# Performance work log

Measured on AMD Instinct MI355X. Metric: run time of the kernel, lower is better.

Reference implementation:

```python
import jax, jax.numpy as jnp
import numpy as np

TOP_K = 2

def setup_inputs() -> dict:
    key = jax.random.key(0)
    k1, k2 = jax.random.split(key)
    B, S, D, E = 4, 8192, 1024, 64
    hidden_states = jax.random.normal(k1, (B, S, D), dtype=jnp.float32)
    gate_weight = jax.random.normal(k2, (E, D), dtype=jnp.float32) * (1.0 / D ** 0.5)
    return {"hidden_states": hidden_states, "gate_weight": gate_weight}

def reference(hidden_states, gate_weight):
    # router_logits: [B, S, E] = hidden @ W^T
    router_logits = jnp.einsum('bsd,ed->bse', hidden_states, gate_weight)
    # softmax in float32 (matches .float() in torch), cast back to input dtype
    router_probs = jax.nn.softmax(router_logits.astype(jnp.float32), axis=-1).astype(hidden_states.dtype)
    top_k_probs, selected_experts = jax.lax.top_k(router_probs, TOP_K)
    top_k_probs = top_k_probs / (jnp.sum(top_k_probs, axis=-1, keepdims=True) + 1e-08)
    return top_k_probs, selected_experts, router_logits
```

## Files before the change

### kernel.cpp

```cpp
#include <hip/hip_runtime.h>
#include <math.h>


typedef __attribute__((ext_vector_type(8))) short bf16x8;
typedef __attribute__((ext_vector_type(4))) float f32x4;

static constexpr int TOKENS = 32768;
static constexpr int DDIM   = 1024;
static constexpr int NEXP   = 64;
static constexpr size_t OFF_EXP = 65536;
static constexpr size_t OFF_LOG = 131072;

__global__ void w_split3_kernel(const float* __restrict__ w,
                                short* __restrict__ w1,
                                short* __restrict__ w2,
                                short* __restrict__ w3) {
    int idx = blockIdx.x * blockDim.x + threadIdx.x;
    for (int i = idx; i < NEXP * DDIM; i += gridDim.x * blockDim.x) {
        int e = i >> 10, k = i & 1023;
        float f = w[i];
        unsigned u1 = __float_as_uint(f);
        float f1 = __uint_as_float(u1 & 0xffff0000u);
        float r1 = f - f1;
        unsigned u2 = __float_as_uint(r1);
        float f2 = __uint_as_float(u2 & 0xffff0000u);
        float r2 = r1 - f2;
        unsigned u3 = __float_as_uint(r2);
        int n = e >> 4, c = k >> 5;
        int lane = (e & 15) + ((k & 31) >> 3) * 16;
        int j = k & 7;
        size_t dst = ((size_t)(c * 4 + n) * 64 + lane) * 8 + j;
        w1[dst] = (short)(u1 >> 16);
        w2[dst] = (short)(u2 >> 16);
        w3[dst] = (short)(u3 >> 16);
    }
}

__device__ inline void split8(float4 a, float4 b,
                              bf16x8& o1, bf16x8& o2, bf16x8& o3) {
    float f[8] = {a.x, a.y, a.z, a.w, b.x, b.y, b.z, b.w};
#pragma unroll
    for (int j = 0; j < 8; ++j) {
        unsigned u1 = __float_as_uint(f[j]);
        float f1 = __uint_as_float(u1 & 0xffff0000u);
        float r1 = f[j] - f1;
        unsigned u2 = __float_as_uint(r1);
        float f2 = __uint_as_float(u2 & 0xffff0000u);
        float r2 = r1 - f2;
        o1[j] = (short)(u1 >> 16);
        o2[j] = (short)(u2 >> 16);
        o3[j] = (short)(__float_as_uint(r2) >> 16);
    }
}

typedef const __attribute__((address_space(1))) unsigned int* gas1_t;
typedef __attribute__((address_space(3))) unsigned int* las3_t;
__device__ inline void stage16(const void* g, void* l) {
    __builtin_amdgcn_global_load_lds((gas1_t)(uintptr_t)g,
                                     (las3_t)(uintptr_t)l, 16, 0, 0);
}

__global__ __launch_bounds__(512, 2)
void router_mfma_kernel(const float* __restrict__ h,
                        const short* __restrict__ w1,
                        const short* __restrict__ w2,
                        const short* __restrict__ w3,
                        float* __restrict__ out) {
    __shared__ alignas(16) char smem[73728];
    const int tid   = threadIdx.x;
    const int lane  = tid & 63;
    const int wv    = tid >> 6;
    const int khalf = wv & 1;
    const int mg    = wv >> 1;
    const int token0 = blockIdx.x * 128 + mg * 32;
    const int arow  = lane & 15;
    const int ks    = lane >> 4;

    const float* ap0 = h + (size_t)(token0 + arow) * DDIM + khalf * 512 + ks * 8;
    const float* ap1 = ap0 + (size_t)16 * DDIM;

    const short* warr[3] = {w1, w2, w3};
    const char* gsrc[3];
    int ldso[3];
#pragma unroll
    for (int i = 0; i < 3; ++i) {
        int seg = wv * 3 + i;
        int kh = seg & 1;
        int an = seg >> 1;
        int a = an >> 2, n = an & 3;
        gsrc[i] = (const char*)warr[a] + (size_t)(kh * 64 + n) * 1024 + lane * 16;
        ldso[i] = (kh * 12 + a * 4 + n) * 1024;
    }

#define STAGE(bb, cc)                                                      \
    {                                                                      \
        _Pragma("unroll")                                                  \
        for (int i = 0; i < 3; ++i)                                        \
            stage16(gsrc[i] + (size_t)(cc) * 4096,                         \
                    smem + (bb) * 24576 + ldso[i]);                        \
    }

    f32x4 acc[2][4];
#pragma unroll
    for (int m = 0; m < 2; ++m)
#pragma unroll
        for (int n = 0; n < 4; ++n)
#pragma unroll
            for (int r = 0; r < 4; ++r) acc[m][n][r] = 0.0f;

    float4 ringA[2][2][2];

    ringA[0][0][0] = *reinterpret_cast<const float4*>(ap0);
    ringA[0][0][1] = *reinterpret_cast<const float4*>(ap0 + 4);
    ringA[0][1][0] = *reinterpret_cast<const float4*>(ap1);
    ringA[0][1][1] = *reinterpret_cast<const float4*>(ap1 + 4);
    STAGE(0, 0);
    STAGE(1, 1);
    asm volatile("s_waitcnt vmcnt(3)" ::: "memory");
    __builtin_amdgcn_s_barrier();

#pragma unroll
    for (int t = 0; t < 16; ++t) {
        const int slot  = t & 1;
        const int nslot = slot ^ 1;
        if (t + 1 < 16) {
            ringA[nslot][0][0] =
                *reinterpret_cast<const float4*>(ap0 + (t + 1) * 32);
            ringA[nslot][0][1] =
                *reinterpret_cast<const float4*>(ap0 + (t + 1) * 32 + 4);
            ringA[nslot][1][0] =
                *reinterpret_cast<const float4*>(ap1 + (t + 1) * 32);
            ringA[nslot][1][1] =
                *reinterpret_cast<const float4*>(ap1 + (t + 1) * 32 + 4);
        }
        if (t + 2 < 16) STAGE((t + 2) % 3, t + 2);

        bf16x8 A1a, A2a, A3a, A1b, A2b, A3b;
        split8(ringA[slot][0][0], ringA[slot][0][1], A1a, A2a, A3a);
        split8(ringA[slot][1][0], ringA[slot][1][1], A1b, A2b, A3b);

        const char* wb = smem + (t % 3) * 24576 + khalf * 12288 + lane * 16;
#pragma unroll
        for (int n = 0; n < 4; ++n) {
            bf16x8 W1v = *reinterpret_cast<const bf16x8*>(wb + n * 1024);
            bf16x8 W2v = *reinterpret_cast<const bf16x8*>(wb + n * 1024 + 4096);
            bf16x8 W3v = *reinterpret_cast<const bf16x8*>(wb + n * 1024 + 8192);
            f32x4 t0 = acc[0][n];
            t0 = __builtin_amdgcn_mfma_f32_16x16x32_bf16(A3a, W1v, t0, 0, 0, 0);
            t0 = __builtin_amdgcn_mfma_f32_16x16x32_bf16(A1a, W3v, t0, 0, 0, 0);
            t0 = __builtin_amdgcn_mfma_f32_16x16x32_bf16(A2a, W2v, t0, 0, 0, 0);
            t0 = __builtin_amdgcn_mfma_f32_16x16x32_bf16(A2a, W1v, t0, 0, 0, 0);
            t0 = __builtin_amdgcn_mfma_f32_16x16x32_bf16(A1a, W2v, t0, 0, 0, 0);
            t0 = __builtin_amdgcn_mfma_f32_16x16x32_bf16(A1a, W1v, t0, 0, 0, 0);
            acc[0][n] = t0;
            f32x4 t1 = acc[1][n];
            t1 = __builtin_amdgcn_mfma_f32_16x16x32_bf16(A3b, W1v, t1, 0, 0, 0);
            t1 = __builtin_amdgcn_mfma_f32_16x16x32_bf16(A1b, W3v, t1, 0, 0, 0);
            t1 = __builtin_amdgcn_mfma_f32_16x16x32_bf16(A2b, W2v, t1, 0, 0, 0);
            t1 = __builtin_amdgcn_mfma_f32_16x16x32_bf16(A2b, W1v, t1, 0, 0, 0);
            t1 = __builtin_amdgcn_mfma_f32_16x16x32_bf16(A1b, W2v, t1, 0, 0, 0);
            t1 = __builtin_amdgcn_mfma_f32_16x16x32_bf16(A1b, W1v, t1, 0, 0, 0);
            acc[1][n] = t1;
        }

        if (t <= 13) {
            asm volatile("s_waitcnt vmcnt(7)" ::: "memory");
            __builtin_amdgcn_s_barrier();
        } else if (t == 14) {
            asm volatile("s_waitcnt vmcnt(4)" ::: "memory");
            __builtin_amdgcn_s_barrier();
        }
    }

    if (khalf == 1) {
        float* cb = (float*)(smem + 24576) + (size_t)(mg * 64 + lane) * 33;
#pragma unroll
        for (int m = 0; m < 2; ++m)
#pragma unroll
            for (int n = 0; n < 4; ++n)
#pragma unroll
                for (int r = 0; r < 4; ++r)
                    cb[m * 16 + n * 4 + r] = acc[m][n][r];
    }
    __syncthreads();
    if (khalf != 0) return;

    {
        const float* cb = (const float*)(smem + 24576)
                        + (size_t)(mg * 64 + lane) * 33;
#pragma unroll
        for (int m = 0; m < 2; ++m)
#pragma unroll
            for (int n = 0; n < 4; ++n)
#pragma unroll
                for (int r = 0; r < 4; ++r)
                    acc[m][n][r] += cb[m * 16 + n * 4 + r];
    }

    const int rbase = (lane >> 4) * 4;
    const int col   = lane & 15;

#pragma unroll
    for (int m = 0; m < 2; ++m)
#pragma unroll
        for (int n = 0; n < 4; ++n)
#pragma unroll
            for (int r = 0; r < 4; ++r)
                out[OFF_LOG + (size_t)(token0 + m * 16 + rbase + r) * NEXP
                    + n * 16 + col] = acc[m][n][r];

#pragma unroll
    for (int m = 0; m < 2; ++m)
#pragma unroll
    for (int r = 0; r < 4; ++r) {
        const int token = token0 + m * 16 + rbase + r;
        float mx = fmaxf(fmaxf(acc[m][0][r], acc[m][1][r]),
                         fmaxf(acc[m][2][r], acc[m][3][r]));
#pragma unroll
        for (int d = 1; d <= 8; d <<= 1) mx = fmaxf(mx, __shfl_xor(mx, d, 64));

        float p[4];
        float s = 0.0f;
#pragma unroll
        for (int n = 0; n < 4; ++n) { p[n] = expf(acc[m][n][r] - mx); s += p[n]; }
#pragma unroll
        for (int d = 1; d <= 8; d <<= 1) s += __shfl_xor(s, d, 64);

        float v1 = -INFINITY, v2 = -INFINITY;
        int   i1 = NEXP,      i2 = NEXP;
#pragma unroll
        for (int n = 0; n < 4; ++n) {
            float v = p[n];
            int   ei = n * 16 + col;
            if (v > v1)      { v2 = v1; i2 = i1; v1 = v; i1 = ei; }
            else if (v > v2) { v2 = v;  i2 = ei; }
        }

#pragma unroll
        for (int d = 1; d <= 8; d <<= 1) {
            float ov1 = __shfl_xor(v1, d, 64);
            float ov2 = __shfl_xor(v2, d, 64);
            int   oi1 = __shfl_xor(i1, d, 64);
            int   oi2 = __shfl_xor(i2, d, 64);
            bool ofirst = (ov1 > v1) || (ov1 == v1 && oi1 < i1);
            float n1, n2; int ni1, ni2;
            if (ofirst) {
                n1 = ov1; ni1 = oi1;
                bool sec = (v1 > ov2) || (v1 == ov2 && i1 < oi2);
                n2 = sec ? v1 : ov2; ni2 = sec ? i1 : oi2;
            } else {
                n1 = v1; ni1 = i1;
                bool sec = (ov1 > v2) || (ov1 == v2 && oi1 < i2);
                n2 = sec ? ov1 : v2; ni2 = sec ? oi1 : i2;
            }
            v1 = n1; i1 = ni1; v2 = n2; i2 = ni2;
        }

        if (col == 0) {
            float t1 = v1 / s;
            float t2 = v2 / s;
            float dn = t1 + t2 + 1e-8f;
            float2 pr; pr.x = t1 / dn; pr.y = t2 / dn;
            *reinterpret_cast<float2*>(out + (size_t)token * 2) = pr;
            float2 ex; ex.x = (float)i1; ex.y = (float)i2;
            *reinterpret_cast<float2*>(out + OFF_EXP + (size_t)token * 2) = ex;
        }
    }
#undef STAGE
}

extern "C" void kernel_launch(void* const* d_in, const int* in_sizes, int n_in,
                              void* d_out, int out_size, void* d_ws, size_t ws_size,
                              hipStream_t stream) {
    const float* h = (const float*)d_in[0];
    const float* w = (const float*)d_in[1];
    float* out = (float*)d_out;
    short* w1 = (short*)d_ws;
    short* w2 = w1 + (size_t)NEXP * DDIM;
    short* w3 = w2 + (size_t)NEXP * DDIM;
    hipLaunchKernelGGL(w_split3_kernel, dim3(128), dim3(256), 0, stream, w, w1, w2, w3);
    hipLaunchKernelGGL(router_mfma_kernel, dim3(TOKENS / 128), dim3(512), 0, stream,
                       h, w1, w2, w3, out);
}
```

Measured before the change: 52.07 us.

## Split expert columns across waves and halve tokens per block

Each block now handles 64 tokens instead of 128. The waves are split three ways: by k-half, by expert half (ng), and by token group. This halves the accumulator registers per wave, and launch bounds are raised to request more resident blocks. The activation prefetch ring is deepened from two to three stages, aligned with the weight staging. The price is an extra LDS reduction round with a second barrier to gather the expert halves. Each weight stage is now loaded into LDS for every 64 tokens rather than every 128, doubling weight staging traffic.

```diff
diff --git a/kernel.cpp b/kernel.cpp
--- a/kernel.cpp
+++ b/kernel.cpp
@@ -60,7 +60,7 @@
                                      (las3_t)(uintptr_t)l, 16, 0, 0);
 }
 
-__global__ __launch_bounds__(512, 2)
+__global__ __launch_bounds__(512, 4)
 void router_mfma_kernel(const float* __restrict__ h,
                         const short* __restrict__ w1,
                         const short* __restrict__ w2,
@@ -71,8 +71,9 @@
     const int lane  = tid & 63;
     const int wv    = tid >> 6;
     const int khalf = wv & 1;
-    const int mg    = wv >> 1;
-    const int token0 = blockIdx.x * 128 + mg * 32;
+    const int ng    = (wv >> 1) & 1;
+    const int mg    = wv >> 2;
+    const int token0 = blockIdx.x * 64 + mg * 32;
     const int arow  = lane & 15;
     const int ks    = lane >> 4;
 
@@ -100,101 +101,129 @@
                     smem + (bb) * 24576 + ldso[i]);                        \
     }
 
-    f32x4 acc[2][4];
+    f32x4 acc[2][2];
 #pragma unroll
     for (int m = 0; m < 2; ++m)
 #pragma unroll
-        for (int n = 0; n < 4; ++n)
-#pragma unroll
-            for (int r = 0; r < 4; ++r) acc[m][n][r] = 0.0f;
-
-    float4 ringA[2][2][2];
-
-    ringA[0][0][0] = *reinterpret_cast<const float4*>(ap0);
-    ringA[0][0][1] = *reinterpret_cast<const float4*>(ap0 + 4);
-    ringA[0][1][0] = *reinterpret_cast<const float4*>(ap1);
-    ringA[0][1][1] = *reinterpret_cast<const float4*>(ap1 + 4);
+        for (int nl = 0; nl < 2; ++nl)
+#pragma unroll
+            for (int r = 0; r < 4; ++r) acc[m][nl][r] = 0.0f;
+
+    float4 ring[3][2][2];
+
     STAGE(0, 0);
     STAGE(1, 1);
-    asm volatile("s_waitcnt vmcnt(3)" ::: "memory");
+    ring[0][0][0] = *reinterpret_cast<const float4*>(ap0);
+    ring[0][0][1] = *reinterpret_cast<const float4*>(ap0 + 4);
+    ring[0][1][0] = *reinterpret_cast<const float4*>(ap1);
+    ring[0][1][1] = *reinterpret_cast<const float4*>(ap1 + 4);
+    ring[1][0][0] = *reinterpret_cast<const float4*>(ap0 + 32);
+    ring[1][0][1] = *reinterpret_cast<const float4*>(ap0 + 36);
+    ring[1][1][0] = *reinterpret_cast<const float4*>(ap1 + 32);
+    ring[1][1][1] = *reinterpret_cast<const float4*>(ap1 + 36);
+    asm volatile("s_waitcnt vmcnt(0)" ::: "memory");
     __builtin_amdgcn_s_barrier();
 
 #pragma unroll
     for (int t = 0; t < 16; ++t) {
-        const int slot  = t & 1;
-        const int nslot = slot ^ 1;
-        if (t + 1 < 16) {
-            ringA[nslot][0][0] =
-                *reinterpret_cast<const float4*>(ap0 + (t + 1) * 32);
-            ringA[nslot][0][1] =
-                *reinterpret_cast<const float4*>(ap0 + (t + 1) * 32 + 4);
-            ringA[nslot][1][0] =
-                *reinterpret_cast<const float4*>(ap1 + (t + 1) * 32);
-            ringA[nslot][1][1] =
-                *reinterpret_cast<const float4*>(ap1 + (t + 1) * 32 + 4);
-        }
-        if (t + 2 < 16) STAGE((t + 2) % 3, t + 2);
+        if (t + 2 < 16) {
+            STAGE((t + 2) % 3, t + 2);
+            ring[(t + 2) % 3][0][0] =
+                *reinterpret_cast<const float4*>(ap0 + (t + 2) * 32);
+            ring[(t + 2) % 3][0][1] =
+                *reinterpret_cast<const float4*>(ap0 + (t + 2) * 32 + 4);
+            ring[(t + 2) % 3][1][0] =
+                *reinterpret_cast<const float4*>(ap1 + (t + 2) * 32);
+            ring[(t + 2) % 3][1][1] =
+                *reinterpret_cast<const float4*>(ap1 + (t + 2) * 32 + 4);
+        }
 
         bf16x8 A1a, A2a, A3a, A1b, A2b, A3b;
-        split8(ringA[slot][0][0], ringA[slot][0][1], A1a, A2a, A3a);
-        split8(ringA[slot][1][0], ringA[slot][1][1], A1b, A2b, A3b);
-
-        const char* wb = smem + (t % 3) * 24576 + khalf * 12288 + lane * 16;
-#pragma unroll
-        for (int n = 0; n < 4; ++n) {
-            bf16x8 W1v = *reinterpret_cast<const bf16x8*>(wb + n * 1024);
-            bf16x8 W2v = *reinterpret_cast<const bf16x8*>(wb + n * 1024 + 4096);
-            bf16x8 W3v = *reinterpret_cast<const bf16x8*>(wb + n * 1024 + 8192);
-            f32x4 t0 = acc[0][n];
+        split8(ring[t % 3][0][0], ring[t % 3][0][1], A1a, A2a, A3a);
+        split8(ring[t % 3][1][0], ring[t % 3][1][1], A1b, A2b, A3b);
+
+        const char* wb = smem + (t % 3) * 24576 + khalf * 12288
+                       + (ng * 2) * 1024 + lane * 16;
+#pragma unroll
+        for (int nl = 0; nl < 2; ++nl) {
+            bf16x8 W1v = *reinterpret_cast<const bf16x8*>(wb + nl * 1024);
+            bf16x8 W2v = *reinterpret_cast<const bf16x8*>(wb + nl * 1024 + 4096);
+            bf16x8 W3v = *reinterpret_cast<const bf16x8*>(wb + nl * 1024 + 8192);
+            f32x4 t0 = acc[0][nl];
             t0 = __builtin_amdgcn_mfma_f32_16x16x32_bf16(A3a, W1v, t0, 0, 0, 0);
             t0 = __builtin_amdgcn_mfma_f32_16x16x32_bf16(A1a, W3v, t0, 0, 0, 0);
             t0 = __builtin_amdgcn_mfma_f32_16x16x32_bf16(A2a, W2v, t0, 0, 0, 0);
             t0 = __builtin_amdgcn_mfma_f32_16x16x32_bf16(A2a, W1v, t0, 0, 0, 0);
             t0 = __builtin_amdgcn_mfma_f32_16x16x32_bf16(A1a, W2v, t0, 0, 0, 0);
             t0 = __builtin_amdgcn_mfma_f32_16x16x32_bf16(A1a, W1v, t0, 0, 0, 0);
-            acc[0][n] = t0;
-            f32x4 t1 = acc[1][n];
+            acc[0][nl] = t0;
+            f32x4 t1 = acc[1][nl];
             t1 = __builtin_amdgcn_mfma_f32_16x16x32_bf16(A3b, W1v, t1, 0, 0, 0);
             t1 = __builtin_amdgcn_mfma_f32_16x16x32_bf16(A1b, W3v, t1, 0, 0, 0);
             t1 = __builtin_amdgcn_mfma_f32_16x16x32_bf16(A2b, W2v, t1, 0, 0, 0);
             t1 = __builtin_amdgcn_mfma_f32_16x16x32_bf16(A2b, W1v, t1, 0, 0, 0);
             t1 = __builtin_amdgcn_mfma_f32_16x16x32_bf16(A1b, W2v, t1, 0, 0, 0);
             t1 = __builtin_amdgcn_mfma_f32_16x16x32_bf16(A1b, W1v, t1, 0, 0, 0);
-            acc[1][n] = t1;
+            acc[1][nl] = t1;
         }
 
         if (t <= 13) {
             asm volatile("s_waitcnt vmcnt(7)" ::: "memory");
             __builtin_amdgcn_s_barrier();
         } else if (t == 14) {
-            asm volatile("s_waitcnt vmcnt(4)" ::: "memory");
+            asm volatile("s_waitcnt vmcnt(0)" ::: "memory");
             __builtin_amdgcn_s_barrier();
         }
     }
 
     if (khalf == 1) {
-        float* cb = (float*)(smem + 24576) + (size_t)(mg * 64 + lane) * 33;
+        float* cA = (float*)(smem + 24576)
+                  + (size_t)((mg * 2 + ng) * 64 + lane) * 17;
 #pragma unroll
         for (int m = 0; m < 2; ++m)
 #pragma unroll
-            for (int n = 0; n < 4; ++n)
+            for (int nl = 0; nl < 2; ++nl)
 #pragma unroll
                 for (int r = 0; r < 4; ++r)
-                    cb[m * 16 + n * 4 + r] = acc[m][n][r];
+                    cA[(m * 2 + nl) * 4 + r] = acc[m][nl][r];
     }
     __syncthreads();
-    if (khalf != 0) return;
-
+    if (khalf == 0) {
+        const float* cA = (const float*)(smem + 24576)
+                        + (size_t)((mg * 2 + ng) * 64 + lane) * 17;
+#pragma unroll
+        for (int m = 0; m < 2; ++m)
+#pragma unroll
+            for (int nl = 0; nl < 2; ++nl)
+#pragma unroll
+                for (int r = 0; r < 4; ++r)
+                    acc[m][nl][r] += cA[(m * 2 + nl) * 4 + r];
+        if (ng == 1) {
+            float* cB = (float*)smem + (size_t)(mg * 64 + lane) * 17;
+#pragma unroll
+            for (int m = 0; m < 2; ++m)
+#pragma unroll
+                for (int nl = 0; nl < 2; ++nl)
+#pragma unroll
+                    for (int r = 0; r < 4; ++r)
+                        cB[(m * 2 + nl) * 4 + r] = acc[m][nl][r];
+        }
+    }
+    __syncthreads();
+    if (khalf != 0 || ng != 0) return;
+
+    f32x4 acc4[2][4];
     {
-        const float* cb = (const float*)(smem + 24576)
-                        + (size_t)(mg * 64 + lane) * 33;
+        const float* cB = (const float*)smem + (size_t)(mg * 64 + lane) * 17;
 #pragma unroll
         for (int m = 0; m < 2; ++m)
 #pragma unroll
-            for (int n = 0; n < 4; ++n)
+            for (int nl = 0; nl < 2; ++nl) {
+                acc4[m][nl] = acc[m][nl];
 #pragma unroll
                 for (int r = 0; r < 4; ++r)
-                    acc[m][n][r] += cb[m * 16 + n * 4 + r];
+                    acc4[m][2 + nl][r] = cB[(m * 2 + nl) * 4 + r];
+            }
     }
 
     const int rbase = (lane >> 4) * 4;
@@ -207,22 +236,22 @@
 #pragma unroll
             for (int r = 0; r < 4; ++r)
                 out[OFF_LOG + (size_t)(token0 + m * 16 + rbase + r) * NEXP
-                    + n * 16 + col] = acc[m][n][r];
+                    + n * 16 + col] = acc4[m][n][r];
 
 #pragma unroll
     for (int m = 0; m < 2; ++m)
 #pragma unroll
     for (int r = 0; r < 4; ++r) {
         const int token = token0 + m * 16 + rbase + r;
-        float mx = fmaxf(fmaxf(acc[m][0][r], acc[m][1][r]),
-                         fmaxf(acc[m][2][r], acc[m][3][r]));
+        float mx = fmaxf(fmaxf(acc4[m][0][r], acc4[m][1][r]),
+                         fmaxf(acc4[m][2][r], acc4[m][3][r]));
 #pragma unroll
         for (int d = 1; d <= 8; d <<= 1) mx = fmaxf(mx, __shfl_xor(mx, d, 64));
 
         float p[4];
         float s = 0.0f;
 #pragma unroll
-        for (int n = 0; n < 4; ++n) { p[n] = expf(acc[m][n][r] - mx); s += p[n]; }
+        for (int n = 0; n < 4; ++n) { p[n] = expf(acc4[m][n][r] - mx); s += p[n]; }
 #pragma unroll
         for (int d = 1; d <= 8; d <<= 1) s += __shfl_xor(s, d, 64);
 
@@ -279,6 +308,6 @@
     short* w2 = w1 + (size_t)NEXP * DDIM;
     short* w3 = w2 + (size_t)NEXP * DDIM;
     hipLaunchKernelGGL(w_split3_kernel, dim3(128), dim3(256), 0, stream, w, w1, w2, w3);
-    hipLaunchKernelGGL(router_mfma_kernel, dim3(TOKENS / 128), dim3(512), 0, stream,
+    hipLaunchKernelGGL(router_mfma_kernel, dim3(TOKENS / 64), dim3(512), 0, stream,
                        h, w1, w2, w3, out);
 }
```

Measured after the change: 62.11 us. 1.19x slower.
